# Optimization experiments

Hardware: AMD Instinct MI355X
Metric: run time of the kernel (lower is better)

## Reference

```python
import jax, jax.numpy as jnp
import numpy as np

N = 3000          # num_nodes
B = 1             # batch
T_IN = 12
T_OUT = 12
F_IN = 2
F_OUT = 2
HEADS = 8
HID = 32          # hidden_dim (GAT out channels, LSTM hidden)
E = 32000         # directed edges (before self-loops)
NEG_SLOPE = 0.2   # PyG GATConv leaky_relu slope


def setup_inputs() -> dict:
    key = jax.random.key(0)
    ks = jax.random.split(key, 20)
    s = 0.1
    inp = {
        "X": jax.random.normal(ks[0], (B, N, T_IN, F_IN), jnp.float32),
        "edge_index": jax.random.randint(ks[1], (2, E), 0, N, dtype=jnp.int64),
        # GATConv params (shared lin for src/dst, concat=False -> bias of size HID)
        "gat_w": jax.random.normal(ks[2], (HEADS * HID, F_IN), jnp.float32) * s,
        "att_src": jax.random.normal(ks[3], (HEADS, HID), jnp.float32) * s,
        "att_dst": jax.random.normal(ks[4], (HEADS, HID), jnp.float32) * s,
        "gat_b": jax.random.normal(ks[5], (HID,), jnp.float32) * s,
        # 2-layer LSTM, PyTorch gate order (i, f, g, o)
        "w_ih0": jax.random.normal(ks[6], (4 * HID, HID), jnp.float32) * s,
        "w_hh0": jax.random.normal(ks[7], (4 * HID, HID), jnp.float32) * s,
        "b_ih0": jax.random.normal(ks[8], (4 * HID,), jnp.float32) * s,
        "b_hh0": jax.random.normal(ks[9], (4 * HID,), jnp.float32) * s,
        "w_ih1": jax.random.normal(ks[10], (4 * HID, HID), jnp.float32) * s,
        "w_hh1": jax.random.normal(ks[11], (4 * HID, HID), jnp.float32) * s,
        "b_ih1": jax.random.normal(ks[12], (4 * HID,), jnp.float32) * s,
        "b_hh1": jax.random.normal(ks[13], (4 * HID,), jnp.float32) * s,
        # final head: HID -> F_OUT * T_OUT
        "fc_w": jax.random.normal(ks[14], (F_OUT * T_OUT, HID), jnp.float32) * s,
        "fc_b": jax.random.normal(ks[15], (F_OUT * T_OUT,), jnp.float32) * s,
    }
    return inp


def _lstm_layer(xs, w_ih, w_hh, b_ih, b_hh):
    # xs: (T, BN, D) -> hidden states (T, BN, H)
    Hd = w_hh.shape[1]
    def step(carry, x):
        h, c = carry
        g = x @ w_ih.T + h @ w_hh.T + b_ih + b_hh
        i, f, gg, o = jnp.split(g, 4, axis=-1)
        c = jax.nn.sigmoid(f) * c + jax.nn.sigmoid(i) * jnp.tanh(gg)
        h = jax.nn.sigmoid(o) * jnp.tanh(c)
        return (h, c), h
    z = jnp.zeros((xs.shape[1], Hd), xs.dtype)
    _, hs = jax.lax.scan(step, (z, z), xs)
    return hs


def reference(X, edge_index, gat_w, att_src, att_dst, gat_b,
              w_ih0, w_hh0, b_ih0, b_hh0, w_ih1, w_hh1, b_ih1, b_hh1,
              fc_w, fc_b):
    Bb, Nn, T, F = X.shape
    BN = Bb * Nn
    H, C = att_src.shape

    # (T, BN, F), all timesteps processed at once (GAT params shared across t)
    Xr = X.transpose(2, 0, 1, 3).reshape(T, BN, F)
    h = (Xr @ gat_w.T).reshape(T, BN, H, C)          # shared lin for src/dst
    a_s = (h * att_src).sum(-1)                      # (T, BN, H)
    a_d = (h * att_dst).sum(-1)

    # add self-loops (PyG GATConv default) over all BN nodes
    loops = jnp.arange(BN, dtype=edge_index.dtype)
    src = jnp.concatenate([edge_index[0], loops])
    dst = jnp.concatenate([edge_index[1], loops])

    # edge attention logits, edge axis leading for segment ops: (Etot, T, H)
    e = jax.nn.leaky_relu(a_s[:, src] + a_d[:, dst], NEG_SLOPE)
    e = jnp.moveaxis(e, 1, 0)

    # segment softmax over incoming edges per destination node
    m = jax.ops.segment_max(e, dst, num_segments=BN)
    ex = jnp.exp(e - m[dst])
    den = jax.ops.segment_sum(ex, dst, num_segments=BN)
    alpha = ex / den[dst]                            # (Etot, T, H)

    h_node = jnp.moveaxis(h, 0, 1)                   # (BN, T, H, C)
    msg = alpha[..., None] * h_node[src]             # (Etot, T, H, C)
    agg = jax.ops.segment_sum(msg, dst, num_segments=BN)  # (BN, T, H, C)
    gat_out = agg.mean(2) + gat_b                    # concat=False -> head mean; (BN, T, C)

    # 2-layer LSTM over time
    xs = gat_out.transpose(1, 0, 2)                  # (T, BN, C)
    hs = _lstm_layer(xs, w_ih0, w_hh0, b_ih0, b_hh0)
    hs = _lstm_layer(hs, w_ih1, w_hh1, b_ih1, b_hh1)
    h_last = hs[-1]                                  # (BN, HID)

    out = h_last @ fc_w.T + fc_b                     # (BN, F_OUT*T_OUT)
    return out.reshape(Bb, Nn, T_OUT, F)
```

## Files before the change

### kernel.cpp

```cpp
#include <hip/hip_runtime.h>
#include <math.h>

#define N_NODES 3000
#define T_STEPS 12
#define F_INP 2
#define HEADS 8
#define HID 32
#define E_EDGES 32000
#define E_TOT (E_EDGES + N_NODES)
#define NEG_SLOPE 0.2f
#define OUT_F 24
#define CHUNKS 8

__device__ __forceinline__ float sigm(float x) {
    return 1.0f / (1.0f + __expf(-x));
}
__device__ __forceinline__ float tanh_f(float x) {
    return 1.0f - 2.0f / (__expf(2.0f * x) + 1.0f);
}
__device__ __forceinline__ float rdlane(float v, int l) {
    return __int_as_float(__builtin_amdgcn_readlane(__float_as_int(v), l));
}

__global__ void k_init(int* __restrict__ deg,
                       const float* __restrict__ gat_w,
                       const float* __restrict__ att_src,
                       const float* __restrict__ att_dst,
                       float* __restrict__ proj) {
    if (blockIdx.x < 12) {
        int i = blockIdx.x * 256 + threadIdx.x;
        if (i < N_NODES) deg[i] = 0;
    } else {
        int tid = threadIdx.x;
        if (tid < 32) {
            int h = tid & 7, w = tid >> 3;
            const float* att = (w < 2) ? att_src : att_dst;
            int f = w & 1;
            float s = 0.0f;
            for (int c = 0; c < 32; c++)
                s += gat_w[((h * 32 + c) * 2) + f] * att[h * 32 + c];
            proj[w * 8 + h] = s;
        }
    }
}

__global__ void k_deg(const int* __restrict__ ei, int* __restrict__ deg) {
    int i = blockIdx.x * blockDim.x + threadIdx.x;
    if (i >= E_TOT) return;
    int d = (i < E_EDGES) ? ei[E_EDGES + i] : (i - E_EDGES);
    atomicAdd(&deg[d], 1);
}

__global__ __launch_bounds__(256) void k_scan(const int* __restrict__ deg,
                                              int* __restrict__ row_start,
                                              int* __restrict__ cursor) {
    __shared__ int part[256];
    int tid = threadIdx.x;
    const int CH = (N_NODES + 255) / 256;
    int base = tid * CH;
    int s = 0;
    for (int i = 0; i < CH; i++) {
        int idx = base + i;
        if (idx < N_NODES) s += deg[idx];
    }
    part[tid] = s;
    __syncthreads();
    if (tid == 0) {
        int run = 0;
        for (int i = 0; i < 256; i++) { int tmp = part[i]; part[i] = run; run += tmp; }
        row_start[N_NODES] = run;
    }
    __syncthreads();
    int off = part[tid];
    for (int i = 0; i < CH; i++) {
        int idx = base + i;
        if (idx < N_NODES) {
            row_start[idx] = off;
            cursor[idx] = off;
            off += deg[idx];
        }
    }
}

__global__ void k_scatter(const int* __restrict__ ei, int* __restrict__ cursor,
                          int* __restrict__ csr_src) {
    int i = blockIdx.x * blockDim.x + threadIdx.x;
    if (i >= E_TOT) return;
    int s, d;
    if (i < E_EDGES) { s = ei[i]; d = ei[E_EDGES + i]; }
    else             { s = i - E_EDGES; d = s; }
    int pos = atomicAdd(&cursor[d], 1);
    csr_src[pos] = s;
}

__global__ __launch_bounds__(256) void k_gat(const float* __restrict__ X,
                                             const int* __restrict__ row_start,
                                             const int* __restrict__ csr_src,
                                             const float* __restrict__ proj,
                                             const float* __restrict__ gat_w,
                                             const float* __restrict__ gat_b,
                                             float* __restrict__ gat_out) {
    int pair = blockIdx.x * 4 + (threadIdx.x >> 6);
    int t = pair / N_NODES, n = pair - t * N_NODES;
    int lane = threadIdx.x & 63;
    int h = lane >> 3, slot = lane & 7;
    int rs = row_start[n];
    int deg = row_start[n + 1] - rs;
    float ps0 = proj[h], ps1 = proj[8 + h];
    float pd0 = proj[16 + h], pd1 = proj[24 + h];
    float xd0 = X[(n * T_STEPS + t) * F_INP + 0];
    float xd1 = X[(n * T_STEPS + t) * F_INP + 1];
    float ad = fmaf(xd0, pd0, xd1 * pd1);

    float x0c[CHUNKS], x1c[CHUNKS], sc[CHUNKS];
    float m = -1e30f;
    #pragma unroll
    for (int c = 0; c < CHUNKS; c++) {
        if (8 * c < deg) {
            int e = slot + 8 * c;
            int idx = rs + (e < deg ? e : deg - 1);
            int src = csr_src[idx];
            float2 xv = *(const float2*)&X[(src * T_STEPS + t) * F_INP];
            x0c[c] = xv.x; x1c[c] = xv.y;
            float s = fmaf(xv.x, ps0, fmaf(xv.y, ps1, ad));
            s = (s > 0.0f) ? s : NEG_SLOPE * s;
            sc[c] = (e < deg) ? s : -1e30f;
            m = fmaxf(m, sc[c]);
        } else { x0c[c] = 0.0f; x1c[c] = 0.0f; sc[c] = -1e30f; }
    }
    for (int e = 64 + slot; e < deg; e += 8) {
        int src = csr_src[rs + e];
        float2 xv = *(const float2*)&X[(src * T_STEPS + t) * F_INP];
        float s = fmaf(xv.x, ps0, fmaf(xv.y, ps1, ad));
        s = (s > 0.0f) ? s : NEG_SLOPE * s;
        m = fmaxf(m, s);
    }
    m = fmaxf(m, __shfl_xor(m, 1, 64));
    m = fmaxf(m, __shfl_xor(m, 2, 64));
    m = fmaxf(m, __shfl_xor(m, 4, 64));

    float den = 0.0f, S0 = 0.0f, S1 = 0.0f;
    #pragma unroll
    for (int c = 0; c < CHUNKS; c++) {
        if (8 * c < deg) {
            float a = __expf(sc[c] - m);
            den += a;
            S0 = fmaf(a, x0c[c], S0);
            S1 = fmaf(a, x1c[c], S1);
        }
    }
    for (int e = 64 + slot; e < deg; e += 8) {
        int src = csr_src[rs + e];
        float2 xv = *(const float2*)&X[(src * T_STEPS + t) * F_INP];
        float s = fmaf(xv.x, ps0, fmaf(xv.y, ps1, ad));
        s = (s > 0.0f) ? s : NEG_SLOPE * s;
        float a = __expf(s - m);
        den += a; S0 = fmaf(a, xv.x, S0); S1 = fmaf(a, xv.y, S1);
    }
    #pragma unroll
    for (int mm = 1; mm <= 4; mm <<= 1) {
        den += __shfl_xor(den, mm, 64);
        S0  += __shfl_xor(S0,  mm, 64);
        S1  += __shfl_xor(S1,  mm, 64);
    }
    float inv = 0.125f / den;
    float v0 = S0 * inv, v1 = S1 * inv;

    float a0[HEADS], a1[HEADS];
    #pragma unroll
    for (int hh = 0; hh < HEADS; hh++) {
        a0[hh] = rdlane(v0, hh * 8);
        a1[hh] = rdlane(v1, hh * 8);
    }

    int cc = lane & 31;
    float acc = gat_b[cc];
    #pragma unroll
    for (int hh = 0; hh < HEADS; hh++) {
        float2 g = *(const float2*)&gat_w[(hh * 32 + cc) * 2];
        acc = fmaf(a0[hh], g.x, fmaf(a1[hh], g.y, acc));
    }
    if (lane < 32)
        gat_out[((size_t)n * T_STEPS + t) * HID + cc] = acc;
}

__global__ __launch_bounds__(64) void k_lstm(const float* __restrict__ xs,
                                             const float* __restrict__ w_ih0,
                                             const float* __restrict__ w_hh0,
                                             const float* __restrict__ b_ih0,
                                             const float* __restrict__ b_hh0,
                                             const float* __restrict__ w_ih1,
                                             const float* __restrict__ w_hh1,
                                             const float* __restrict__ b_ih1,
                                             const float* __restrict__ b_hh1,
                                             const float* __restrict__ fc_w,
                                             const float* __restrict__ fc_b,
                                             float* __restrict__ out) {
    int n = blockIdx.x;
    int lane = threadIdx.x;
    int j = lane & 31, half = lane >> 5;
    int rowA = half * 64 + j;
    int rowB = half * 64 + 32 + j;

    float wA[32], wB[32];
    #pragma unroll
    for (int q = 0; q < 8; q++) {
        float4 va = *(const float4*)&w_ih0[rowA * 32 + 4 * q];
        float4 vb = *(const float4*)&w_ih0[rowB * 32 + 4 * q];
        wA[4*q] = va.x; wA[4*q+1] = va.y; wA[4*q+2] = va.z; wA[4*q+3] = va.w;
        wB[4*q] = vb.x; wB[4*q+1] = vb.y; wB[4*q+2] = vb.z; wB[4*q+3] = vb.w;
    }
    float bA = b_ih0[rowA] + b_hh0[rowA];
    float bB = b_ih0[rowB] + b_hh0[rowB];

    float xrow[T_STEPS];
    #pragma unroll
    for (int t = 0; t < T_STEPS; t++)
        xrow[t] = xs[((size_t)n * T_STEPS + t) * HID + j];

    float gxa[T_STEPS], gxb[T_STEPS];
    #pragma unroll
    for (int t = 0; t < T_STEPS; t++) {
        float a = bA, b = bB;
        #pragma unroll
        for (int k = 0; k < 32; k++) {
            float xk = rdlane(xrow[t], k);
            a = fmaf(xk, wA[k], a);
            b = fmaf(xk, wB[k], b);
        }
        gxa[t] = a; gxb[t] = b;
    }
    #pragma unroll
    for (int q = 0; q < 8; q++) {
        float4 va = *(const float4*)&w_hh0[rowA * 32 + 4 * q];
        float4 vb = *(const float4*)&w_hh0[rowB * 32 + 4 * q];
        wA[4*q] = va.x; wA[4*q+1] = va.y; wA[4*q+2] = va.z; wA[4*q+3] = va.w;
        wB[4*q] = vb.x; wB[4*q+1] = vb.y; wB[4*q+2] = vb.z; wB[4*q+3] = vb.w;
    }
    float h = 0.0f, c = 0.0f;
    float h0s[T_STEPS];
    #pragma unroll
    for (int t = 0; t < T_STEPS; t++) {
        float gA = gxa[t], gB = gxb[t];
        #pragma unroll
        for (int k = 0; k < 32; k++) {
            float hk = rdlane(h, k);
            gA = fmaf(hk, wA[k], gA);
            gB = fmaf(hk, wB[k], gB);
        }
        float oA = __shfl_xor(gA, 32, 64);
        float oB = __shfl_xor(gB, 32, 64);
        float gi = half ? oA : gA;
        float gf = half ? oB : gB;
        float gg = half ? gA : oA;
        float go = half ? gB : oB;
        c = sigm(gf) * c + sigm(gi) * tanh_f(gg);
        h = sigm(go) * tanh_f(c);
        h0s[t] = h;
    }
    float bA1 = b_ih1[rowA] + b_hh1[rowA];
    float bB1 = b_ih1[rowB] + b_hh1[rowB];
    #pragma unroll
    for (int q = 0; q < 8; q++) {
        float4 va = *(const float4*)&w_ih1[rowA * 32 + 4 * q];
        float4 vb = *(const float4*)&w_ih1[rowB * 32 + 4 * q];
        wA[4*q] = va.x; wA[4*q+1] = va.y; wA[4*q+2] = va.z; wA[4*q+3] = va.w;
        wB[4*q] = vb.x; wB[4*q+1] = vb.y; wB[4*q+2] = vb.z; wB[4*q+3] = vb.w;
    }
    #pragma unroll
    for (int t = 0; t < T_STEPS; t++) {
        float a = bA1, b = bB1;
        #pragma unroll
        for (int k = 0; k < 32; k++) {
            float xk = rdlane(h0s[t], k);
            a = fmaf(xk, wA[k], a);
            b = fmaf(xk, wB[k], b);
        }
        gxa[t] = a; gxb[t] = b;
    }
    #pragma unroll
    for (int q = 0; q < 8; q++) {
        float4 va = *(const float4*)&w_hh1[rowA * 32 + 4 * q];
        float4 vb = *(const float4*)&w_hh1[rowB * 32 + 4 * q];
        wA[4*q] = va.x; wA[4*q+1] = va.y; wA[4*q+2] = va.z; wA[4*q+3] = va.w;
        wB[4*q] = vb.x; wB[4*q+1] = vb.y; wB[4*q+2] = vb.z; wB[4*q+3] = vb.w;
    }
    h = 0.0f; c = 0.0f;
    #pragma unroll
    for (int t = 0; t < T_STEPS; t++) {
        float gA = gxa[t], gB = gxb[t];
        #pragma unroll
        for (int k = 0; k < 32; k++) {
            float hk = rdlane(h, k);
            gA = fmaf(hk, wA[k], gA);
            gB = fmaf(hk, wB[k], gB);
        }
        float oA = __shfl_xor(gA, 32, 64);
        float oB = __shfl_xor(gB, 32, 64);
        float gi = half ? oA : gA;
        float gf = half ? oB : gB;
        float gg = half ? gA : oA;
        float go = half ? gB : oB;
        c = sigm(gf) * c + sigm(gi) * tanh_f(gg);
        h = sigm(go) * tanh_f(c);
    }
    int o = (lane < OUT_F) ? lane : (OUT_F - 1);
    float fw[32];
    #pragma unroll
    for (int q = 0; q < 8; q++) {
        float4 v = *(const float4*)&fc_w[o * 32 + 4 * q];
        fw[4*q] = v.x; fw[4*q+1] = v.y; fw[4*q+2] = v.z; fw[4*q+3] = v.w;
    }
    float acc = fc_b[o];
    #pragma unroll
    for (int k = 0; k < 32; k++) {
        float hk = rdlane(h, k);
        acc = fmaf(hk, fw[k], acc);
    }
    if (lane < OUT_F) out[(size_t)n * OUT_F + lane] = acc;
}

extern "C" void kernel_launch(void* const* d_in, const int* in_sizes, int n_in,
                              void* d_out, int out_size, void* d_ws, size_t ws_size,
                              hipStream_t stream) {
    (void)in_sizes; (void)n_in; (void)out_size; (void)ws_size;
    const float* X       = (const float*)d_in[0];
    const int*   ei      = (const int*)d_in[1];
    const float* gat_w   = (const float*)d_in[2];
    const float* att_src = (const float*)d_in[3];
    const float* att_dst = (const float*)d_in[4];
    const float* gat_b   = (const float*)d_in[5];
    const float* w_ih0   = (const float*)d_in[6];
    const float* w_hh0   = (const float*)d_in[7];
    const float* b_ih0   = (const float*)d_in[8];
    const float* b_hh0   = (const float*)d_in[9];
    const float* w_ih1   = (const float*)d_in[10];
    const float* w_hh1   = (const float*)d_in[11];
    const float* b_ih1   = (const float*)d_in[12];
    const float* b_hh1   = (const float*)d_in[13];
    const float* fc_w    = (const float*)d_in[14];
    const float* fc_b    = (const float*)d_in[15];
    float* out = (float*)d_out;

    char* ws = (char*)d_ws;
    size_t off = 0;
    auto alloc_f = [&](size_t n) { float* p = (float*)(ws + off); off += n * sizeof(float); return p; };
    auto alloc_i = [&](size_t n) { int* p = (int*)(ws + off); off += n * sizeof(int); return p; };

    float* gat_out = alloc_f((size_t)N_NODES * T_STEPS * HID);
    float* proj    = alloc_f(32);
    int* deg       = alloc_i(N_NODES);
    int* row_start = alloc_i(N_NODES + 1);
    int* cursor    = alloc_i(N_NODES);
    int* csr_src   = alloc_i(E_TOT);

    k_init<<<13, 256, 0, stream>>>(deg, gat_w, att_src, att_dst, proj);
    k_deg<<<(E_TOT + 255) / 256, 256, 0, stream>>>(ei, deg);
    k_scan<<<1, 256, 0, stream>>>(deg, row_start, cursor);
    k_scatter<<<(E_TOT + 255) / 256, 256, 0, stream>>>(ei, cursor, csr_src);
    k_gat<<<(T_STEPS * N_NODES) / 4, 256, 0, stream>>>(X, row_start, csr_src, proj,
                                                       gat_w, gat_b, gat_out);
    k_lstm<<<N_NODES, 64, 0, stream>>>(gat_out, w_ih0, w_hh0, b_ih0, b_hh0,
                                       w_ih1, w_hh1, b_ih1, b_hh1,
                                       fc_w, fc_b, out);
}
```

Before: 167.8 us.

## Transpose X to time-major, split LSTM layer-0 input projection into separate kernel

The init kernel now transposes X into a time-major float2 array, so the GAT gather reads a compact per-timestep slice. The layer-0 input projection moves out of the per-node LSTM kernel into a new highly parallel kernel that writes gx0 to workspace. The recurrent dot products are split into two accumulator chains to shorten FMA dependency latency, and the LSTM kernel gets a launch-bounds occupancy hint. In exchange there is an extra kernel launch and an extra global round trip for the 128-wide gate pre-activations.

```diff
diff --git a/kernel.cpp b/kernel.cpp
--- a/kernel.cpp
+++ b/kernel.cpp
@@ -11,6 +11,7 @@
 #define NEG_SLOPE 0.2f
 #define OUT_F 24
 #define CHUNKS 8
+#define NT (N_NODES * T_STEPS)
 
 __device__ __forceinline__ float sigm(float x) {
     return 1.0f / (1.0f + __expf(-x));
@@ -26,11 +27,14 @@
                        const float* __restrict__ gat_w,
                        const float* __restrict__ att_src,
                        const float* __restrict__ att_dst,
-                       float* __restrict__ proj) {
-    if (blockIdx.x < 12) {
-        int i = blockIdx.x * 256 + threadIdx.x;
+                       float* __restrict__ proj,
+                       const float* __restrict__ X,
+                       float2* __restrict__ Xt) {
+    int b = blockIdx.x;
+    if (b < 12) {
+        int i = b * 256 + threadIdx.x;
         if (i < N_NODES) deg[i] = 0;
-    } else {
+    } else if (b == 12) {
         int tid = threadIdx.x;
         if (tid < 32) {
             int h = tid & 7, w = tid >> 3;
@@ -40,6 +44,13 @@
             for (int c = 0; c < 32; c++)
                 s += gat_w[((h * 32 + c) * 2) + f] * att[h * 32 + c];
             proj[w * 8 + h] = s;
+        }
+    } else {
+        int i = (b - 13) * 256 + threadIdx.x;
+        if (i < NT) {
+            int n = i / T_STEPS, t = i - n * T_STEPS;
+            float2 v = *(const float2*)&X[(size_t)i * 2];
+            Xt[(size_t)t * N_NODES + n] = v;
         }
     }
 }
@@ -93,7 +104,7 @@
     csr_src[pos] = s;
 }
 
-__global__ __launch_bounds__(256) void k_gat(const float* __restrict__ X,
+__global__ __launch_bounds__(256) void k_gat(const float2* __restrict__ Xt,
                                              const int* __restrict__ row_start,
                                              const int* __restrict__ csr_src,
                                              const float* __restrict__ proj,
@@ -106,11 +117,11 @@
     int h = lane >> 3, slot = lane & 7;
     int rs = row_start[n];
     int deg = row_start[n + 1] - rs;
+    const float2* Xp = Xt + (size_t)t * N_NODES;
     float ps0 = proj[h], ps1 = proj[8 + h];
     float pd0 = proj[16 + h], pd1 = proj[24 + h];
-    float xd0 = X[(n * T_STEPS + t) * F_INP + 0];
-    float xd1 = X[(n * T_STEPS + t) * F_INP + 1];
-    float ad = fmaf(xd0, pd0, xd1 * pd1);
+    float2 xd = Xp[n];
+    float ad = fmaf(xd.x, pd0, xd.y * pd1);
 
     float x0c[CHUNKS], x1c[CHUNKS], sc[CHUNKS];
     float m = -1e30f;
@@ -120,7 +131,7 @@
             int e = slot + 8 * c;
             int idx = rs + (e < deg ? e : deg - 1);
             int src = csr_src[idx];
-            float2 xv = *(const float2*)&X[(src * T_STEPS + t) * F_INP];
+            float2 xv = Xp[src];
             x0c[c] = xv.x; x1c[c] = xv.y;
             float s = fmaf(xv.x, ps0, fmaf(xv.y, ps1, ad));
             s = (s > 0.0f) ? s : NEG_SLOPE * s;
@@ -129,8 +140,7 @@
         } else { x0c[c] = 0.0f; x1c[c] = 0.0f; sc[c] = -1e30f; }
     }
     for (int e = 64 + slot; e < deg; e += 8) {
-        int src = csr_src[rs + e];
-        float2 xv = *(const float2*)&X[(src * T_STEPS + t) * F_INP];
+        float2 xv = Xp[csr_src[rs + e]];
         float s = fmaf(xv.x, ps0, fmaf(xv.y, ps1, ad));
         s = (s > 0.0f) ? s : NEG_SLOPE * s;
         m = fmaxf(m, s);
@@ -150,8 +160,7 @@
         }
     }
     for (int e = 64 + slot; e < deg; e += 8) {
-        int src = csr_src[rs + e];
-        float2 xv = *(const float2*)&X[(src * T_STEPS + t) * F_INP];
+        float2 xv = Xp[csr_src[rs + e]];
         float s = fmaf(xv.x, ps0, fmaf(xv.y, ps1, ad));
         s = (s > 0.0f) ? s : NEG_SLOPE * s;
         float a = __expf(s - m);
@@ -184,18 +193,37 @@
         gat_out[((size_t)n * T_STEPS + t) * HID + cc] = acc;
 }
 
-__global__ __launch_bounds__(64) void k_lstm(const float* __restrict__ xs,
-                                             const float* __restrict__ w_ih0,
-                                             const float* __restrict__ w_hh0,
-                                             const float* __restrict__ b_ih0,
-                                             const float* __restrict__ b_hh0,
-                                             const float* __restrict__ w_ih1,
-                                             const float* __restrict__ w_hh1,
-                                             const float* __restrict__ b_ih1,
-                                             const float* __restrict__ b_hh1,
-                                             const float* __restrict__ fc_w,
-                                             const float* __restrict__ fc_b,
-                                             float* __restrict__ out) {
+__global__ __launch_bounds__(256) void k_proj0(const float* __restrict__ gat_out,
+                                               const float* __restrict__ w_ih0,
+                                               const float* __restrict__ b_ih0,
+                                               const float* __restrict__ b_hh0,
+                                               float* __restrict__ gx0) {
+    int p = blockIdx.x * 2 + (threadIdx.x >> 7);
+    int r = threadIdx.x & 127;
+    const float* x = &gat_out[(size_t)p * HID];
+    float acc = b_ih0[r] + b_hh0[r];
+    #pragma unroll
+    for (int q = 0; q < 8; q++) {
+        float4 xv = *(const float4*)&x[4 * q];
+        float4 wv = *(const float4*)&w_ih0[r * 32 + 4 * q];
+        acc = fmaf(xv.x, wv.x, acc);
+        acc = fmaf(xv.y, wv.y, acc);
+        acc = fmaf(xv.z, wv.z, acc);
+        acc = fmaf(xv.w, wv.w, acc);
+    }
+    gx0[(size_t)p * 128 + r] = acc;
+}
+
+__global__ __launch_bounds__(64, 3)
+void k_lstm(const float* __restrict__ gx0,
+            const float* __restrict__ w_hh0,
+            const float* __restrict__ w_ih1,
+            const float* __restrict__ w_hh1,
+            const float* __restrict__ b_ih1,
+            const float* __restrict__ b_hh1,
+            const float* __restrict__ fc_w,
+            const float* __restrict__ fc_b,
+            float* __restrict__ out) {
     int n = blockIdx.x;
     int lane = threadIdx.x;
     int j = lane & 31, half = lane >> 5;
@@ -205,49 +233,25 @@
     float wA[32], wB[32];
     #pragma unroll
     for (int q = 0; q < 8; q++) {
-        float4 va = *(const float4*)&w_ih0[rowA * 32 + 4 * q];
-        float4 vb = *(const float4*)&w_ih0[rowB * 32 + 4 * q];
-        wA[4*q] = va.x; wA[4*q+1] = va.y; wA[4*q+2] = va.z; wA[4*q+3] = va.w;
-        wB[4*q] = vb.x; wB[4*q+1] = vb.y; wB[4*q+2] = vb.z; wB[4*q+3] = vb.w;
-    }
-    float bA = b_ih0[rowA] + b_hh0[rowA];
-    float bB = b_ih0[rowB] + b_hh0[rowB];
-
-    float xrow[T_STEPS];
-    #pragma unroll
-    for (int t = 0; t < T_STEPS; t++)
-        xrow[t] = xs[((size_t)n * T_STEPS + t) * HID + j];
-
-    float gxa[T_STEPS], gxb[T_STEPS];
-    #pragma unroll
-    for (int t = 0; t < T_STEPS; t++) {
-        float a = bA, b = bB;
-        #pragma unroll
-        for (int k = 0; k < 32; k++) {
-            float xk = rdlane(xrow[t], k);
-            a = fmaf(xk, wA[k], a);
-            b = fmaf(xk, wB[k], b);
-        }
-        gxa[t] = a; gxb[t] = b;
-    }
-    #pragma unroll
-    for (int q = 0; q < 8; q++) {
         float4 va = *(const float4*)&w_hh0[rowA * 32 + 4 * q];
         float4 vb = *(const float4*)&w_hh0[rowB * 32 + 4 * q];
         wA[4*q] = va.x; wA[4*q+1] = va.y; wA[4*q+2] = va.z; wA[4*q+3] = va.w;
         wB[4*q] = vb.x; wB[4*q+1] = vb.y; wB[4*q+2] = vb.z; wB[4*q+3] = vb.w;
     }
+
     float h = 0.0f, c = 0.0f;
     float h0s[T_STEPS];
     #pragma unroll
     for (int t = 0; t < T_STEPS; t++) {
-        float gA = gxa[t], gB = gxb[t];
+        const float* g = &gx0[((size_t)n * T_STEPS + t) * 128];
+        float gA0 = g[rowA], gB0 = g[rowB], gA1 = 0.0f, gB1 = 0.0f;
         #pragma unroll
-        for (int k = 0; k < 32; k++) {
-            float hk = rdlane(h, k);
-            gA = fmaf(hk, wA[k], gA);
-            gB = fmaf(hk, wB[k], gB);
-        }
+        for (int k = 0; k < 16; k++) {
+            float h0 = rdlane(h, k), h1 = rdlane(h, k + 16);
+            gA0 = fmaf(h0, wA[k], gA0);      gA1 = fmaf(h1, wA[k + 16], gA1);
+            gB0 = fmaf(h0, wB[k], gB0);      gB1 = fmaf(h1, wB[k + 16], gB1);
+        }
+        float gA = gA0 + gA1, gB = gB0 + gB1;
         float oA = __shfl_xor(gA, 32, 64);
         float oB = __shfl_xor(gB, 32, 64);
         float gi = half ? oA : gA;
@@ -258,8 +262,6 @@
         h = sigm(go) * tanh_f(c);
         h0s[t] = h;
     }
-    float bA1 = b_ih1[rowA] + b_hh1[rowA];
-    float bB1 = b_ih1[rowB] + b_hh1[rowB];
     #pragma unroll
     for (int q = 0; q < 8; q++) {
         float4 va = *(const float4*)&w_ih1[rowA * 32 + 4 * q];
@@ -267,6 +269,9 @@
         wA[4*q] = va.x; wA[4*q+1] = va.y; wA[4*q+2] = va.z; wA[4*q+3] = va.w;
         wB[4*q] = vb.x; wB[4*q+1] = vb.y; wB[4*q+2] = vb.z; wB[4*q+3] = vb.w;
     }
+    float bA1 = b_ih1[rowA] + b_hh1[rowA];
+    float bB1 = b_ih1[rowB] + b_hh1[rowB];
+    float gxa1[T_STEPS], gxb1[T_STEPS];
     #pragma unroll
     for (int t = 0; t < T_STEPS; t++) {
         float a = bA1, b = bB1;
@@ -276,7 +281,7 @@
             a = fmaf(xk, wA[k], a);
             b = fmaf(xk, wB[k], b);
         }
-        gxa[t] = a; gxb[t] = b;
+        gxa1[t] = a; gxb1[t] = b;
     }
     #pragma unroll
     for (int q = 0; q < 8; q++) {
@@ -288,13 +293,14 @@
     h = 0.0f; c = 0.0f;
     #pragma unroll
     for (int t = 0; t < T_STEPS; t++) {
-        float gA = gxa[t], gB = gxb[t];
+        float gA0 = gxa1[t], gB0 = gxb1[t], gA1 = 0.0f, gB1 = 0.0f;
         #pragma unroll
-        for (int k = 0; k < 32; k++) {
-            float hk = rdlane(h, k);
-            gA = fmaf(hk, wA[k], gA);
-            gB = fmaf(hk, wB[k], gB);
-        }
+        for (int k = 0; k < 16; k++) {
+            float h0 = rdlane(h, k), h1 = rdlane(h, k + 16);
+            gA0 = fmaf(h0, wA[k], gA0);      gA1 = fmaf(h1, wA[k + 16], gA1);
+            gB0 = fmaf(h0, wB[k], gB0);      gB1 = fmaf(h1, wB[k + 16], gB1);
+        }
+        float gA = gA0 + gA1, gB = gB0 + gB1;
         float oA = __shfl_xor(gA, 32, 64);
         float oB = __shfl_xor(gB, 32, 64);
         float gi = half ? oA : gA;
@@ -347,20 +353,23 @@
     auto alloc_f = [&](size_t n) { float* p = (float*)(ws + off); off += n * sizeof(float); return p; };
     auto alloc_i = [&](size_t n) { int* p = (int*)(ws + off); off += n * sizeof(int); return p; };
 
-    float* gat_out = alloc_f((size_t)N_NODES * T_STEPS * HID);
-    float* proj    = alloc_f(32);
+    float*  gat_out = alloc_f((size_t)NT * HID);
+    float*  gx0     = alloc_f((size_t)NT * 128);
+    float2* Xt      = (float2*)alloc_f((size_t)NT * 2);
+    float*  proj    = alloc_f(32);
     int* deg       = alloc_i(N_NODES);
     int* row_start = alloc_i(N_NODES + 1);
     int* cursor    = alloc_i(N_NODES);
     int* csr_src   = alloc_i(E_TOT);
 
-    k_init<<<13, 256, 0, stream>>>(deg, gat_w, att_src, att_dst, proj);
+    k_init<<<13 + (NT + 255) / 256, 256, 0, stream>>>(deg, gat_w, att_src, att_dst,
+                                                      proj, X, Xt);
     k_deg<<<(E_TOT + 255) / 256, 256, 0, stream>>>(ei, deg);
     k_scan<<<1, 256, 0, stream>>>(deg, row_start, cursor);
     k_scatter<<<(E_TOT + 255) / 256, 256, 0, stream>>>(ei, cursor, csr_src);
-    k_gat<<<(T_STEPS * N_NODES) / 4, 256, 0, stream>>>(X, row_start, csr_src, proj,
-                                                       gat_w, gat_b, gat_out);
-    k_lstm<<<N_NODES, 64, 0, stream>>>(gat_out, w_ih0, w_hh0, b_ih0, b_hh0,
-                                       w_ih1, w_hh1, b_ih1, b_hh1,
+    k_gat<<<NT / 4, 256, 0, stream>>>(Xt, row_start, csr_src, proj,
+                                      gat_w, gat_b, gat_out);
+    k_proj0<<<NT / 2, 256, 0, stream>>>(gat_out, w_ih0, b_ih0, b_hh0, gx0);
+    k_lstm<<<N_NODES, 64, 0, stream>>>(gx0, w_hh0, w_ih1, w_hh1, b_ih1, b_hh1,
                                        fc_w, fc_b, out);
 }
```

Measured after the change: 258.1 us. 1.54x slower.
